# Performance work log

Measured on AMD Instinct MI355X. Metric: run time of the kernel, lower is better.

Reference implementation:

```python
import jax, jax.numpy as jnp
import numpy as np
from functools import partial

B, L, V = 64, 512, 20000
P, M = 150, 6          # total patterns, max pattern length
NEG = -1e9             # semiring zero (log-space)
END_STATES = np.repeat(np.array([3, 4, 5]), 50)  # pattern_len-1 per pattern


@jax.custom_vjp
def ste_heaviside(x):
    return (x > 0).astype(x.dtype)

def _ste_fwd(x):
    return ste_heaviside(x), None

def _ste_bwd(_, g):
    return (g,)  # straight-through identity (matches torch code path)

ste_heaviside.defvjp(_ste_fwd, _ste_bwd)


def setup_inputs() -> dict:
    key = jax.random.key(0)
    ks = jax.random.split(key, 8)
    return {
        "docs": jax.random.randint(ks[0], (B, L), 0, V),
        "doc_lens": jax.random.randint(ks[1], (B,), 1, L),
        "local_embeddings": jax.random.normal(ks[2], (300, V), jnp.float32),
        "diags": jax.random.normal(ks[3], (P * M, 300), jnp.float32) * 0.05,
        "bias": jax.random.normal(ks[4], (P * M, 1), jnp.float32) * 0.05,
        "wildcards": jax.random.normal(ks[5], (P, M - 1), jnp.float32) * 0.05,
        "ln_gamma": jnp.ones((P,), jnp.float32),
        "ln_beta": jnp.zeros((P,), jnp.float32),
        "linear_w": jax.random.normal(ks[6], (2, P), jnp.float32) * 0.05,
        "linear_b": jnp.zeros((2,), jnp.float32),
    }


def reference(docs, doc_lens, local_embeddings, diags, bias, wildcards,
              ln_gamma, ln_beta, linear_w, linear_b):
    end_states = jnp.asarray(END_STATES)                  # [P]
    pat_idx = jnp.arange(P)

    # transition matrices over local vocab, mapped into log-space semiring
    tm_vocab = jax.nn.log_sigmoid((diags @ local_embeddings + bias).T)  # [V, P*M]
    tm = tm_vocab[docs].reshape(B, L, P, M)               # [B,L,P,M]

    # wildcard transitions: semiring.times(one=0, log_sigmoid(wildcards))
    wild = jax.nn.log_sigmoid(wildcards)                  # [P, M-1]

    restart = jnp.zeros((B, P, 1), tm.dtype)              # semiring one
    hid0 = jnp.full((B, P, M), NEG, tm.dtype).at[:, :, 0].set(0.0)
    scores0 = jnp.full((B, P), NEG, tm.dtype)             # semiring zero

    def step(carry, inputs):
        hid, sc = carry
        t, tm_t = inputs                                  # tm_t: [B,P,M]
        main = jnp.concatenate([restart, hid[:, :, :-1] + tm_t[:, :, :-1]], axis=2)
        wildp = jnp.concatenate([restart, hid[:, :, :-1] + wild[None]], axis=2)
        hid = jnp.maximum(main, wildp)                    # semiring plus
        esv = hid[:, pat_idx, end_states]                 # [B,P]
        active = (doc_lens > t)[:, None]
        sc = jnp.where(active, jnp.maximum(sc, esv), sc)
        return (hid, sc), None

    xs = (jnp.arange(L), jnp.moveaxis(tm, 1, 0))          # [L], [L,B,P,M]
    (_, scores), _ = jax.lax.scan(step, (hid0, scores0), xs)

    scores = jnp.exp(scores)                              # from_semiring_to_outer
    mu = scores.mean(axis=-1, keepdims=True)
    var = scores.var(axis=-1, keepdims=True)
    norm = (scores - mu) * jax.lax.rsqrt(var + 1e-5) * ln_gamma + ln_beta
    binar = ste_heaviside(norm)
    return binar @ linear_w.T + linear_b
```

## Files before the change

kernel.cpp:

```cpp
#include <hip/hip_runtime.h>
#include <hip/hip_bf16.h>
#include <hip/hip_fp16.h>
#include <math.h>

#define B_   64
#define L_   512
#define V_   20000
#define P_   150
#define M_   6
#define KDIM 300
#define NOUT 750
#define CWS  752
#define NEGF (-1.0e9f)

#define BM 128
#define BN 128
#define BK 16
#define LDP 132

#define KP 320
#define NIT 10
#define NVG 157
#define NJ  6
#define TILE_U4 1024
#define SA 1024.0f
#define SB 16384.0f
#define INV24 (5.9604644775390625e-8f)

#define TCHUNK 32
#define NCHUNK (L_ / TCHUNK)
#define WARM   5
#define CS_STRIDE 160
#define KVBUF 3

typedef _Float16 f16x8 __attribute__((ext_vector_type(8)));
typedef float f32x16 __attribute__((ext_vector_type(16)));

__device__ __forceinline__ float logsigf(float x) {
    return fminf(x, 0.f) - log1pf(expf(-fabsf(x)));
}

__device__ __forceinline__ float logsigf_fast(float x) {
    return fminf(x, 0.f) - __logf(1.f + __expf(-fabsf(x)));
}

__device__ __forceinline__ void gload_lds16(const void* gp, void* lp) {
    __builtin_amdgcn_global_load_lds(
        (const __attribute__((address_space(1))) unsigned int*)gp,
        (__attribute__((address_space(3))) unsigned int*)lp, 16, 0, 0);
}


__global__ __launch_bounds__(256) void p12_split(
    const float* __restrict__ emb, const float* __restrict__ diags,
    uint4* __restrict__ a_t, uint4* __restrict__ b_t)
{
    __shared__ float T[64][132];
    const int t   = threadIdx.x;
    const int bid = blockIdx.x;

    if (bid < NVG * 5) {
        const int gx = bid % NVG;
        const int ky = bid / NVG;
        const int v0 = gx * 128;
        const int k0 = ky * 64;

        #pragma unroll
        for (int pass = 0; pass < 8; ++pass) {
            int flat = pass * 256 + t;
            int krow = flat >> 5;
            int c4   = (flat & 31) * 4;
            int kg   = k0 + krow;
            int v    = v0 + c4;
            float4 f = {0.f, 0.f, 0.f, 0.f};
            if (kg < KDIM && v + 3 < V_)
                f = *(const float4*)(emb + (size_t)kg * V_ + v);
            *(float4*)&T[krow][c4] = f;
        }
        __syncthreads();

        const int vv = t >> 1;
        const int kh = (t & 1) * 32;
        const int it = ky * 2 + (kh >> 5);
        const int v  = v0 + vv;
        if (v < V_) {
            union { ushort u[8]; uint4 q; } H[4], Lo[4];
            #pragma unroll
            for (int i = 0; i < 32; ++i) {
                float x = T[kh + i][vv] * SA;
                __half h = __float2half_rn(x);
                float rem = x - __half2float(h);
                H[i >> 3].u[i & 7]  = __half_as_ushort(h);
                Lo[i >> 3].u[i & 7] = __half_as_ushort(__float2half_rn(rem));
            }
            uint4* tile = a_t + ((size_t)gx * NIT + it) * TILE_U4;
            #pragma unroll
            for (int c = 0; c < 4; ++c) {
                tile[      c * 128 + vv] = H[c].q;
                tile[512 + c * 128 + vv] = Lo[c].q;
            }
        }
    } else {
        const int bidx = bid - NVG * 5;
        const int it   = bidx % NIT;
        const int j    = bidx / NIT;
        const int row  = t >> 1;
        const int qh   = (t & 1) * 2;
        const int n    = j * 128 + row;
        const bool nok = (n < NOUT);
        const int pm   = nok ? ((n / 5) * 6 + (n % 5)) : 0;
        uint4* tile = b_t + (size_t)bidx * TILE_U4;
        #pragma unroll
        for (int qq = 0; qq < 2; ++qq) {
            int q = qh + qq;
            union { ushort u[8]; uint4 v; } H, Lo;
            #pragma unroll
            for (int e = 0; e < 8; ++e) {
                int k = it * 32 + q * 8 + e;
                float x = (nok && k < KDIM) ? diags[(size_t)pm * KDIM + k] * SB : 0.f;
                __half h = __float2half_rn(x);
                float rem = x - __half2float(h);
                H.u[e]  = __half_as_ushort(h);
                Lo.u[e] = __half_as_ushort(__float2half_rn(rem));
            }
            tile[      q * 128 + row] = H.v;
            tile[512 + q * 128 + row] = Lo.v;
        }
    }
}

__global__ __launch_bounds__(512) void k1m_gemm(
    const uint4* __restrict__ a_t, const uint4* __restrict__ b_t,
    const float* __restrict__ bias, const float* __restrict__ wildc,
    float* __restrict__ cw)
{
    const int bid = blockIdx.x;
    const int c   = bid / 24;
    const int r   = bid % 24;
    const int gp  = c * 8 + (r & 7);
    const int h   = r >> 3;
    if (gp >= 79) return;

    __shared__ uint4 sm[2][4096];
    const int t    = threadIdx.x;
    const int lane = t & 63;
    const int w    = t >> 6;
    const int wr   = w >> 2;
    const int wc   = w & 3;
    const int fk16 = lane >> 5;
    const int fm   = lane & 31;

    const int ga = 2 * gp;
    const int gb = (2 * gp + 1 < NVG) ? (2 * gp + 1) : (NVG - 1);
    const uint4* abase0 = a_t + (size_t)ga * NIT * TILE_U4;
    const uint4* abase1 = a_t + (size_t)gb * NIT * TILE_U4;
    const uint4* bbase0 = b_t + (size_t)(2 * h)     * NIT * TILE_U4;
    const uint4* bbase1 = b_t + (size_t)(2 * h + 1) * NIT * TILE_U4;

    f32x16 acc[4][2];
    #pragma unroll
    for (int i = 0; i < 4; ++i)
        #pragma unroll
        for (int jj = 0; jj < 2; ++jj)
            #pragma unroll
            for (int e = 0; e < 16; ++e) acc[i][jj][e] = 0.f;

    uint4 rg[8];

    #define LOAD_SET(IT)                                   \
        do {                                               \
            const size_t o = (size_t)(IT) * TILE_U4;       \
            rg[0] = abase0[o + t];                         \
            rg[1] = abase0[o + 512 + t];                   \
            rg[2] = abase1[o + t];                         \
            rg[3] = abase1[o + 512 + t];                   \
            rg[4] = bbase0[o + t];                         \
            rg[5] = bbase0[o + 512 + t];                   \
            rg[6] = bbase1[o + t];                         \
            rg[7] = bbase1[o + 512 + t];                   \
        } while (0)

    #define WRITE_SET(BSEL)                                \
        do {                                               \
            uint4* smb = &sm[(BSEL)][0];                   \
            smb[        t] = rg[0];                        \
            smb[ 512 +  t] = rg[1];                        \
            smb[1024 +  t] = rg[2];                        \
            smb[1536 +  t] = rg[3];                        \
            smb[2048 +  t] = rg[4];                        \
            smb[2560 +  t] = rg[5];                        \
            smb[3072 +  t] = rg[6];                        \
            smb[3584 +  t] = rg[7];                        \
        } while (0)

    LOAD_SET(0);
    WRITE_SET(0);
    LOAD_SET(1);
    __syncthreads();

    #pragma unroll
    for (int it = 0; it < NIT; ++it) {
        if (it + 1 < NIT) WRITE_SET((it + 1) & 1);
        if (it + 2 < NIT) LOAD_SET(it + 2);

        const uint4* smc = &sm[it & 1][0];
        #pragma unroll
        for (int s = 0; s < 2; ++s) {
            const int q = s * 2 + fk16;
            f16x8 A1[4], A2[4], B1[2], B2[2];
            #pragma unroll
            for (int ri = 0; ri < 4; ++ri) {
                const int ao = wr * 1024 + q * 128 + ri * 32 + fm;
                A1[ri] = *(const f16x8*)&smc[ao];
                A2[ri] = *(const f16x8*)&smc[ao + 512];
            }
            #pragma unroll
            for (int cj = 0; cj < 2; ++cj) {
                const int colb = wc * 64 + cj * 32;
                const int bo = 2048 + (colb >> 7) * 1024 + q * 128 + (colb & 127) + fm;
                B1[cj] = *(const f16x8*)&smc[bo];
                B2[cj] = *(const f16x8*)&smc[bo + 512];
            }
            #pragma unroll
            for (int ri = 0; ri < 4; ++ri)
                #pragma unroll
                for (int cj = 0; cj < 2; ++cj) {
                    acc[ri][cj] = __builtin_amdgcn_mfma_f32_32x32x16_f16(A1[ri], B1[cj], acc[ri][cj], 0, 0, 0);
                    acc[ri][cj] = __builtin_amdgcn_mfma_f32_32x32x16_f16(A1[ri], B2[cj], acc[ri][cj], 0, 0, 0);
                    acc[ri][cj] = __builtin_amdgcn_mfma_f32_32x32x16_f16(A2[ri], B1[cj], acc[ri][cj], 0, 0, 0);
                }
        }

        if (it + 1 < NIT) __syncthreads();
    }
    #undef LOAD_SET
    #undef WRITE_SET

    float biasv[2], lwv[2]; int ncol[2]; bool nok[2];
    #pragma unroll
    for (int cj = 0; cj < 2; ++cj) {
        int n = h * 256 + wc * 64 + cj * 32 + fm;
        ncol[cj] = n;
        nok[cj]  = (n < NOUT);
        int nc = nok[cj] ? n : 0;
        int pm = (nc / 5) * 6 + (nc % 5);
        biasv[cj] = bias[pm];
        lwv[cj]   = logsigf_fast(wildc[nc]);
    }
    const int v0 = gp * 256;
    #pragma unroll
    for (int ri = 0; ri < 4; ++ri) {
        int vbase = v0 + wr * 128 + ri * 32 + 4 * fk16;
        #pragma unroll
        for (int cj = 0; cj < 2; ++cj) {
            if (!nok[cj]) continue;
            #pragma unroll
            for (int e = 0; e < 16; ++e) {
                int v = vbase + (e & 3) + 8 * (e >> 2);
                if (v < V_) {
                    float val = acc[ri][cj][e] * INV24 + biasv[cj];
                    cw[(size_t)v * CWS + ncol[cj]] = fmaxf(logsigf_fast(val), lwv[cj]);
                }
            }
        }
    }
}


__global__ __launch_bounds__(256) void k1_gemm_cw(
    const float* __restrict__ emb,
    const float* __restrict__ diags,
    const float* __restrict__ bias,
    const float* __restrict__ wildc,
    float* __restrict__ cw)
{
    __shared__ float As[BK][LDP];
    __shared__ float Bs[BK][LDP];

    const int tid = threadIdx.x;
    const int v0 = blockIdx.x * BM;
    const int n0 = blockIdx.y * BN;
    const int tx = tid & 15;
    const int ty = tid >> 4;

    float acc[8][8];
    #pragma unroll
    for (int i = 0; i < 8; ++i)
        #pragma unroll
        for (int j = 0; j < 8; ++j) acc[i][j] = 0.f;

    const int a_k = tid >> 4;
    const int a_v = (tid & 15) * 8;
    const int b_n   = tid >> 1;
    const int b_kof = (tid & 1) * 8;

    int  brow;
    bool bval;
    {
        int n = n0 + b_n;
        bval = (n < NOUT);
        brow = bval ? ((n / 5) * 6 + (n % 5)) : 0;
    }

    for (int k0 = 0; k0 < KDIM; k0 += BK) {
        {
            float4 f0 = {0,0,0,0}, f1 = {0,0,0,0};
            int k = k0 + a_k;
            if (k < KDIM) {
                const float* src = emb + (size_t)k * V_ + v0 + a_v;
                if (v0 + a_v + 3 < V_) f0 = *(const float4*)src;
                if (v0 + a_v + 7 < V_) f1 = *(const float4*)(src + 4);
            }
            *(float4*)&As[a_k][a_v]     = f0;
            *(float4*)&As[a_k][a_v + 4] = f1;
        }
        {
            float4 f = {0,0,0,0}, g = {0,0,0,0};
            if (bval) {
                const float* src = diags + (size_t)brow * KDIM + k0 + b_kof;
                if (k0 + b_kof + 3 < KDIM) f = *(const float4*)src;
                if (k0 + b_kof + 7 < KDIM) g = *(const float4*)(src + 4);
            }
            Bs[b_kof + 0][b_n] = f.x;
            Bs[b_kof + 1][b_n] = f.y;
            Bs[b_kof + 2][b_n] = f.z;
            Bs[b_kof + 3][b_n] = f.w;
            Bs[b_kof + 4][b_n] = g.x;
            Bs[b_kof + 5][b_n] = g.y;
            Bs[b_kof + 6][b_n] = g.z;
            Bs[b_kof + 7][b_n] = g.w;
        }
        __syncthreads();
        #pragma unroll
        for (int k = 0; k < BK; ++k) {
            float4 a0 = *(const float4*)&As[k][tx * 4];
            float4 a1 = *(const float4*)&As[k][64 + tx * 4];
            float4 b0 = *(const float4*)&Bs[k][ty * 8];
            float4 b1 = *(const float4*)&Bs[k][ty * 8 + 4];
            float av[8] = {a0.x, a0.y, a0.z, a0.w, a1.x, a1.y, a1.z, a1.w};
            float bv[8] = {b0.x, b0.y, b0.z, b0.w, b1.x, b1.y, b1.z, b1.w};
            #pragma unroll
            for (int i = 0; i < 8; ++i)
                #pragma unroll
                for (int j = 0; j < 8; ++j)
                    acc[i][j] = fmaf(av[i], bv[j], acc[i][j]);
        }
        __syncthreads();
    }

    float biasv[8], lwv[8];
    #pragma unroll
    for (int j = 0; j < 8; ++j) {
        int n  = n0 + ty * 8 + j;
        int nc = (n < NOUT) ? n : 0;
        int pm = (nc / 5) * 6 + (nc % 5);
        biasv[j] = bias[pm];
        lwv[j]   = logsigf(wildc[nc]);
    }
    #pragma unroll
    for (int i = 0; i < 8; ++i) {
        int v = v0 + ((i < 4) ? (tx * 4 + i) : (64 + tx * 4 + (i - 4)));
        if (v >= V_) continue;
        float r[8];
        #pragma unroll
        for (int j = 0; j < 8; ++j)
            r[j] = fmaxf(logsigf(acc[i][j] + biasv[j]), lwv[j]);
        float* dst = cw + (size_t)v * CWS + n0 + ty * 8;
        if (n0 + ty * 8     < NOUT) *(float4*)dst       = make_float4(r[0], r[1], r[2], r[3]);
        if (n0 + ty * 8 + 4 < NOUT) *(float4*)(dst + 4) = make_float4(r[4], r[5], r[6], r[7]);
    }
}


__global__ __launch_bounds__(192) void k2_scan(
    const int* __restrict__ docs,
    const int* __restrict__ doc_lens,
    const float* __restrict__ cw,
    float* __restrict__ cs)
{
    const int ci = blockIdx.x;
    const int b  = blockIdx.y;
    const int t0 = ci * TCHUNK;
    const int ts = (t0 >= WARM) ? (t0 - WARM) : 0;
    const int dl = doc_lens[b];
    const int te = min(t0 + TCHUNK, dl);
    const int nt = te - ts;

    __shared__ int   toks[TCHUNK + WARM];
    __shared__ float rows[KVBUF][3][768];

    const int t    = threadIdx.x;
    const int lane = t & 63;
    const int w    = t >> 6;

    if (t < TCHUNK + WARM) {
        int tt = ts + t;
        toks[t] = docs[b * L_ + min(tt, L_ - 1)];
    }
    __syncthreads();

    const int p      = t;
    const int e      = (p < 50) ? 3 : (p < 100) ? 4 : 5;
    const int warm_n = t0 - ts;
    float h1 = NEGF, h2 = NEGF, h3 = NEGF, h4 = NEGF, h5 = NEGF, sc = NEGF;

    const int nrounds = (nt > 0) ? (nt + 2) / 3 : 0;

    for (int r0 = 0; r0 < 2; ++r0) {
        if (r0 >= nrounds) break;
        int idx = min(3 * r0 + w, nt - 1);
        const char* rowp = (const char*)(cw + (size_t)toks[idx] * CWS);
        char* lbase = (char*)&rows[r0][w][0];
        #pragma unroll
        for (int jj = 0; jj < 3; ++jj)
            gload_lds16(rowp + jj * 1024 + lane * 16,
                        lbase + jj * 1024 + lane * 16);
    }

    int bufc = 0;
    for (int r = 0; r < nrounds; ++r) {
        if (r + 1 < nrounds) {
            asm volatile("s_waitcnt vmcnt(3)" ::: "memory");
        } else {
            asm volatile("s_waitcnt vmcnt(0)" ::: "memory");
        }
        __builtin_amdgcn_s_barrier();
        asm volatile("" ::: "memory");

        if (r + 2 < nrounds) {
            int rn  = r + 2;
            int idx = min(3 * rn + w, nt - 1);
            const char* rowp = (const char*)(cw + (size_t)toks[idx] * CWS);
            int bn = bufc + 2; if (bn >= KVBUF) bn -= KVBUF;
            char* lbase = (char*)&rows[bn][w][0];
            #pragma unroll
            for (int jj = 0; jj < 3; ++jj)
                gload_lds16(rowp + jj * 1024 + lane * 16,
                            lbase + jj * 1024 + lane * 16);
        }

        #pragma unroll
        for (int u = 0; u < 3; ++u) {
            int i2 = 3 * r + u;
            if (i2 >= nt) break;
            if (p < P_) {
                const float* rp = &rows[bufc][u][p * 5];
                float c0 = rp[0], c1 = rp[1], c2 = rp[2], c3 = rp[3], c4 = rp[4];
                h5 = h4 + c4;
                h4 = h3 + c3;
                h3 = h2 + c2;
                h2 = h1 + c1;
                h1 = c0;
                if (i2 >= warm_n) {
                    float esv = (e == 3) ? h3 : (e == 4) ? h4 : h5;
                    sc = fmaxf(sc, esv);
                }
            }
        }
        bufc = (bufc + 1 == KVBUF) ? 0 : bufc + 1;
    }
    if (p < P_) cs[(size_t)(b * NCHUNK + ci) * CS_STRIDE + p] = sc;
}

__device__ __forceinline__ float block_sum192(float v, volatile float* red, int tid) {
    #pragma unroll
    for (int off = 32; off > 0; off >>= 1) v += __shfl_down(v, off, 64);
    __syncthreads();
    if ((tid & 63) == 0) red[tid >> 6] = v;
    __syncthreads();
    return red[0] + red[1] + red[2];
}

__global__ __launch_bounds__(192) void k3_final(
    const float* __restrict__ cs,
    const float* __restrict__ gamma,
    const float* __restrict__ beta,
    const float* __restrict__ lw,
    const float* __restrict__ lb,
    float* __restrict__ out)
{
    __shared__ float red[3];
    const int b   = blockIdx.x;
    const int tid = threadIdx.x;
    float s = 0.f;
    if (tid < P_) {
        float m = NEGF;
        const float* row = cs + (size_t)b * NCHUNK * CS_STRIDE + tid;
        #pragma unroll
        for (int ci = 0; ci < NCHUNK; ++ci) m = fmaxf(m, row[ci * CS_STRIDE]);
        s = expf(m);
    }
    float mu = block_sum192(s, red, tid) * (1.f / P_);
    float d  = (tid < P_) ? (s - mu) : 0.f;
    float var = block_sum192(d * d, red, tid) * (1.f / P_);
    float bin = 0.f;
    if (tid < P_) {
        float norm = (s - mu) * rsqrtf(var + 1e-5f) * gamma[tid] + beta[tid];
        bin = (norm > 0.f) ? 1.f : 0.f;
    }
    float o0 = block_sum192((tid < P_) ? bin * lw[tid]      : 0.f, red, tid);
    float o1 = block_sum192((tid < P_) ? bin * lw[P_ + tid] : 0.f, red, tid);
    if (tid == 0) {
        out[b * 2 + 0] = o0 + lb[0];
        out[b * 2 + 1] = o1 + lb[1];
    }
}

extern "C" void kernel_launch(void* const* d_in, const int* in_sizes, int n_in,
                              void* d_out, int out_size, void* d_ws, size_t ws_size,
                              hipStream_t stream)
{
    const int*   docs  = (const int*)  d_in[0];
    const int*   dlens = (const int*)  d_in[1];
    const float* emb   = (const float*)d_in[2];
    const float* diags = (const float*)d_in[3];
    const float* bias  = (const float*)d_in[4];
    const float* wildc = (const float*)d_in[5];
    const float* gamma = (const float*)d_in[6];
    const float* beta  = (const float*)d_in[7];
    const float* lw    = (const float*)d_in[8];
    const float* lb    = (const float*)d_in[9];
    float* out = (float*)d_out;

    const size_t cw_b = (size_t)V_ * CWS * 4;
    const size_t cs_b = (size_t)B_ * NCHUNK * CS_STRIDE * 4;
    const size_t at_b = (size_t)NVG * NIT * TILE_U4 * 16;
    const size_t bt_b = (size_t)NJ  * NIT * TILE_U4 * 16;
    const size_t need = cw_b + cs_b + at_b + bt_b;

    char* base = (char*)d_ws;
    float* cw = (float*)base;
    float* cs = (float*)(base + cw_b);
    uint4* at = (uint4*)(base + cw_b + cs_b);
    uint4* bt = (uint4*)(base + cw_b + cs_b + at_b);

    if (ws_size >= need) {
        p12_split<<<NVG * 5 + NJ * NIT, 256, 0, stream>>>(emb, diags, at, bt);
        k1m_gemm<<<240, 512, 0, stream>>>(at, bt, bias, wildc, cw);
    } else {
        dim3 g1((V_ + BM - 1) / BM, (NOUT + BN - 1) / BN);
        k1_gemm_cw<<<g1, 256, 0, stream>>>(emb, diags, bias, wildc, cw);
    }

    dim3 g2(NCHUNK, B_);
    k2_scan<<<g2, 192, 0, stream>>>(docs, dlens, cw, cs);
    k3_final<<<B_, 192, 0, stream>>>(cs, gamma, beta, lw, lb, out);
}
```

Measured before the change: 178.6 us.

## Stream GEMM tiles directly from global memory into LDS, bypassing registers

The register-staged double buffer in the vocab-projection GEMM is replaced with direct global-to-LDS loads via gload_lds16. Each wave now copies one 512-element section of the A or B tile. The loop issues the next tile's loads after a barrier at the top of each iteration. This frees the eight uint4 staging registers and the explicit LDS write pass, and the kernel is pinned to 2 waves per EU. In exchange the prefetch distance drops from two iterations to one. Correctness relies on the barrier also waiting for the outstanding direct-to-LDS loads.

Result: faster. 148.5 us (-16.9%).

```diff
diff --git a/kernel.cpp b/kernel.cpp
--- a/kernel.cpp
+++ b/kernel.cpp
@@ -129,7 +129,8 @@
     }
 }
 
-__global__ __launch_bounds__(512) void k1m_gemm(
+__global__ __attribute__((amdgpu_waves_per_eu(2, 2))) __launch_bounds__(512)
+void k1m_gemm(
     const uint4* __restrict__ a_t, const uint4* __restrict__ b_t,
     const float* __restrict__ bias, const float* __restrict__ wildc,
     float* __restrict__ cw)
@@ -152,10 +153,13 @@
 
     const int ga = 2 * gp;
     const int gb = (2 * gp + 1 < NVG) ? (2 * gp + 1) : (NVG - 1);
-    const uint4* abase0 = a_t + (size_t)ga * NIT * TILE_U4;
-    const uint4* abase1 = a_t + (size_t)gb * NIT * TILE_U4;
-    const uint4* bbase0 = b_t + (size_t)(2 * h)     * NIT * TILE_U4;
-    const uint4* bbase1 = b_t + (size_t)(2 * h + 1) * NIT * TILE_U4;
+    const int sel  = w >> 1;
+    const int half = w & 1;
+    const uint4* gsec =
+        ((sel == 0) ? a_t + (size_t)ga * NIT * TILE_U4 :
+         (sel == 1) ? a_t + (size_t)gb * NIT * TILE_U4 :
+         (sel == 2) ? b_t + (size_t)(2 * h)     * NIT * TILE_U4 :
+                      b_t + (size_t)(2 * h + 1) * NIT * TILE_U4) + half * 512;
 
     f32x16 acc[4][2];
     #pragma unroll
@@ -165,45 +169,25 @@
             #pragma unroll
             for (int e = 0; e < 16; ++e) acc[i][jj][e] = 0.f;
 
-    uint4 rg[8];
-
-    #define LOAD_SET(IT)                                   \
-        do {                                               \
-            const size_t o = (size_t)(IT) * TILE_U4;       \
-            rg[0] = abase0[o + t];                         \
-            rg[1] = abase0[o + 512 + t];                   \
-            rg[2] = abase1[o + t];                         \
-            rg[3] = abase1[o + 512 + t];                   \
-            rg[4] = bbase0[o + t];                         \
-            rg[5] = bbase0[o + 512 + t];                   \
-            rg[6] = bbase1[o + t];                         \
-            rg[7] = bbase1[o + 512 + t];                   \
-        } while (0)
-
-    #define WRITE_SET(BSEL)                                \
-        do {                                               \
-            uint4* smb = &sm[(BSEL)][0];                   \
-            smb[        t] = rg[0];                        \
-            smb[ 512 +  t] = rg[1];                        \
-            smb[1024 +  t] = rg[2];                        \
-            smb[1536 +  t] = rg[3];                        \
-            smb[2048 +  t] = rg[4];                        \
-            smb[2560 +  t] = rg[5];                        \
-            smb[3072 +  t] = rg[6];                        \
-            smb[3584 +  t] = rg[7];                        \
-        } while (0)
-
-    LOAD_SET(0);
-    WRITE_SET(0);
-    LOAD_SET(1);
-    __syncthreads();
-
-    #pragma unroll
+    {
+        const uint4* gp0 = gsec + lane;
+        #pragma unroll
+        for (int i = 0; i < 8; ++i)
+            gload_lds16(gp0 + i * 64, &sm[0][w * 512 + i * 64 + lane]);
+    }
+
+    int cur = 0;
     for (int it = 0; it < NIT; ++it) {
-        if (it + 1 < NIT) WRITE_SET((it + 1) & 1);
-        if (it + 2 < NIT) LOAD_SET(it + 2);
-
-        const uint4* smc = &sm[it & 1][0];
+        __syncthreads();
+
+        if (it + 1 < NIT) {
+            const uint4* gpp = gsec + (size_t)(it + 1) * TILE_U4 + lane;
+            #pragma unroll
+            for (int i = 0; i < 8; ++i)
+                gload_lds16(gpp + i * 64, &sm[cur ^ 1][w * 512 + i * 64 + lane]);
+        }
+
+        const uint4* smc = &sm[cur][0];
         #pragma unroll
         for (int s = 0; s < 2; ++s) {
             const int q = s * 2 + fk16;
@@ -230,11 +214,8 @@
                     acc[ri][cj] = __builtin_amdgcn_mfma_f32_32x32x16_f16(A2[ri], B1[cj], acc[ri][cj], 0, 0, 0);
                 }
         }
-
-        if (it + 1 < NIT) __syncthreads();
-    }
-    #undef LOAD_SET
-    #undef WRITE_SET
+        cur ^= 1;
+    }
 
     float biasv[2], lwv[2]; int ncol[2]; bool nok[2];
     #pragma unroll
```
